# Performance work log

Hardware: AMD Instinct MI355X
Metric: run time of the kernel (lower is better)

## Reference

```python
import jax, jax.numpy as jnp
import numpy as np
from functools import partial

DIM = 192
HEADS = 8
DN = ('NCHW', 'OIHW', 'NCHW')


def conv1x1(x, w):
    # w: [O, I, 1, 1]
    return jax.lax.conv_general_dilated(x, w, (1, 1), 'VALID', dimension_numbers=DN)


def dwconv3x3(x, w):
    # w: [C, 1, 3, 3], depthwise
    return jax.lax.conv_general_dilated(x, w, (1, 1), 'SAME', dimension_numbers=DN,
                                        feature_group_count=x.shape[1])


def l2norm(x, eps=1e-12):
    n = jnp.sqrt(jnp.sum(x * x, axis=-1, keepdims=True))
    return x / jnp.maximum(n, eps)


def compute_attention(q, k_s, v_s, k_c, v_c, temperature, beta):
    b, c, h, w = q.shape
    hw = h * w
    r = lambda t: t.reshape(b, HEADS, c // HEADS, hw)  # b head c (h w)
    qn = l2norm(r(q))
    ks = l2norm(r(k_s))
    kc = l2norm(r(k_c))
    vs, vc = r(v_s), r(v_c)
    # channel-wise attention: [b, head, c, c]
    sa = jax.nn.softmax(jnp.einsum('bhcn,bhdn->bhcd', qn, ks) * temperature, axis=-1)
    so = jnp.einsum('bhcd,bhdn->bhcn', sa, vs)
    ca = jax.nn.softmax(-(jnp.einsum('bhcn,bhdn->bhcd', qn, kc) * temperature), axis=-1)
    co = jnp.einsum('bhcd,bhdn->bhcn', ca, vc)
    out = jax.nn.sigmoid(beta) * so + co
    return out.reshape(b, c, h, w)


def setup_inputs() -> dict:
    key = jax.random.key(0)
    ks = jax.random.split(key, 8)
    B, C, H, W = 8, DIM, 128, 128
    s = 0.02
    return {
        'x1': jax.random.normal(ks[0], (B, C, H, W), jnp.float32),
        'x2': jax.random.normal(ks[1], (B, C, H, W), jnp.float32),
        'w_qkv1': jax.random.normal(ks[2], (3 * C, C, 1, 1), jnp.float32) * s,
        'w_dw1': jax.random.normal(ks[3], (3 * C, 1, 3, 3), jnp.float32) * s,
        'w_qkv2': jax.random.normal(ks[4], (3 * C, C, 1, 1), jnp.float32) * s,
        'w_dw2': jax.random.normal(ks[5], (3 * C, 1, 3, 3), jnp.float32) * s,
        'w_proj': jax.random.normal(ks[6], (C, C, 1, 1), jnp.float32) * s,
        'temperature': jnp.ones((HEADS, 1, 1), jnp.float32),
        'beta': jnp.zeros((1,), jnp.float32),
    }


def reference(x1, x2, w_qkv1, w_dw1, w_qkv2, w_dw2, w_proj, temperature, beta):
    qkv1 = dwconv3x3(conv1x1(x1, w_qkv1), w_dw1)
    q1, k1, v1 = jnp.split(qkv1, 3, axis=1)
    qkv2 = dwconv3x3(conv1x1(x2, w_qkv2), w_dw2)
    q2, k2, v2 = jnp.split(qkv2, 3, axis=1)
    e1 = compute_attention(q1, k1, v1, k2, v2, temperature, beta)
    e2 = compute_attention(q2, k2, v2, k1, v1, temperature, beta)
    return conv1x1(e1, w_proj), conv1x1(e2, w_proj)
```

## Files before the change

### kernel.cpp

```cpp
#include <hip/hip_runtime.h>

typedef unsigned short u16;
typedef unsigned int u32;

#define NB 8
#define NCH 192
#define NC3 576
#define NHW 16384
#define NHEADS 8

typedef __attribute__((ext_vector_type(8))) short s16x8;
typedef __attribute__((ext_vector_type(4))) float f32x4;

__device__ __forceinline__ float bf2f(u32 h) {
  return __uint_as_float(h << 16);
}
__device__ __forceinline__ u16 f2bf(float f) {
  u32 u = __float_as_uint(f);
  u = (u + 0x7fffu + ((u >> 16) & 1u)) >> 16;
  return (u16)u;
}
__device__ __forceinline__ u32 pk2(u16 a, u16 b) { return (u32)a | ((u32)b << 16); }

__device__ __forceinline__ int swz(int row) { return ((row >> 1) & 7) << 4; }

__device__ __forceinline__ void gl_lds16(const void* g, void* s) {
  __builtin_amdgcn_global_load_lds((const __attribute__((address_space(1))) unsigned int*)g,
                                   (__attribute__((address_space(3))) unsigned int*)s, 16, 0, 0);
}

__global__ __launch_bounds__(256) void wcast_kernel(
    const float* __restrict__ w1, const float* __restrict__ w2,
    u16* __restrict__ o1, u16* __restrict__ o2, float* __restrict__ norms2) {
  int i = blockIdx.x * 256 + threadIdx.x;
  if (i < NC3 * NCH) {
    o1[i] = f2bf(w1[i]);
    o2[i] = f2bf(w2[i]);
  }
  if (i < 4 * NB * NCH) norms2[i] = 0.f;
}

__global__ __launch_bounds__(256) void conv_mfma_kernel(
    const float* __restrict__ x, const u16* __restrict__ wbf, u16* __restrict__ pre) {
  __shared__ char smem[40960];
  u16* Al = (u16*)smem;
  u16* Bl = (u16*)(smem + 24576);
  const int bid = blockIdx.x;
  const int id = (bid & 7) * 384 + (bid >> 3);
  const int b = id / 384;
  const int rr = id % 384;
  const int nbase = (rr / 3) * 128;
  const int obase = (rr % 3) * 192;
  const int tid = threadIdx.x;
  const int w = tid >> 6, l = tid & 63;
  const int wr = w >> 1, wc = w & 1;

  f32x4 acc[6][4];
#pragma unroll
  for (int m = 0; m < 6; ++m)
#pragma unroll
    for (int nf = 0; nf < 4; ++nf) acc[m][nf] = (f32x4)0.f;

  for (int kb = 0; kb < 192; kb += 64) {
#pragma unroll
    for (int i = 0; i < 6; ++i) {
      const int grp = i * 4 + w;
      const int row = grp * 8 + (l >> 3);
      const int cb = ((l & 7) * 16) ^ swz(row);
      const char* src = (const char*)wbf + (size_t)(obase + row) * 384 + kb * 2 + cb;
      gl_lds16(src, (char*)Al + grp * 1024);
    }
#pragma unroll
    for (int pi = 0; pi < 2; ++pi) {
      const int p = pi * 256 + tid;
      const int ng = p & 31, kg = p >> 5;
      const float* xr = x + (((size_t)b * NCH + kb + kg * 4) << 14) + nbase + ng * 4;
      float4 f0 = *(const float4*)(xr);
      float4 f1 = *(const float4*)(xr + NHW);
      float4 f2 = *(const float4*)(xr + 2 * NHW);
      float4 f3 = *(const float4*)(xr + 3 * NHW);
      u16 e0[4] = {f2bf(f0.x), f2bf(f0.y), f2bf(f0.z), f2bf(f0.w)};
      u16 e1[4] = {f2bf(f1.x), f2bf(f1.y), f2bf(f1.z), f2bf(f1.w)};
      u16 e2[4] = {f2bf(f2.x), f2bf(f2.y), f2bf(f2.z), f2bf(f2.w)};
      u16 e3[4] = {f2bf(f3.x), f2bf(f3.y), f2bf(f3.z), f2bf(f3.w)};
#pragma unroll
      for (int nn = 0; nn < 4; ++nn) {
        const int row = ng * 4 + nn;
        const int cb = (kg * 8) ^ swz(row);
        *(uint2*)((char*)Bl + row * 128 + cb) = make_uint2(pk2(e0[nn], e1[nn]), pk2(e2[nn], e3[nn]));
      }
    }
    __syncthreads();
#pragma unroll
    for (int kk = 0; kk < 2; ++kk) {
      s16x8 a[6], bv[4];
      const int cbk = kk * 64 + (l >> 4) * 16;
#pragma unroll
      for (int m = 0; m < 6; ++m) {
        const int rowA = wr * 96 + m * 16 + (l & 15);
        a[m] = *(const s16x8*)((const char*)Al + rowA * 128 + (cbk ^ swz(rowA)));
      }
#pragma unroll
      for (int nf = 0; nf < 4; ++nf) {
        const int rowB = wc * 64 + nf * 16 + (l & 15);
        bv[nf] = *(const s16x8*)((const char*)Bl + rowB * 128 + (cbk ^ swz(rowB)));
      }
#pragma unroll
      for (int m = 0; m < 6; ++m)
#pragma unroll
        for (int nf = 0; nf < 4; ++nf)
          acc[m][nf] = __builtin_amdgcn_mfma_f32_16x16x32_bf16(a[m], bv[nf], acc[m][nf], 0, 0, 0);
    }
    __syncthreads();
  }
  u16* cw = (u16*)(smem) + w * 16 * 72;
#pragma unroll
  for (int m = 0; m < 6; ++m) {
#pragma unroll
    for (int nf = 0; nf < 4; ++nf)
#pragma unroll
      for (int r = 0; r < 4; ++r)
        cw[((l >> 4) * 4 + r) * 72 + nf * 16 + (l & 15)] = f2bf(acc[m][nf][r]);
#pragma unroll
    for (int p = 0; p < 2; ++p) {
      const int chunk = p * 64 + l;
      const int row = chunk >> 3, cg = chunk & 7;
      uint4 v = *(const uint4*)(cw + row * 72 + cg * 8);
      const int o = obase + wr * 96 + m * 16 + row;
      const int n = nbase + wc * 64 + cg * 8;
      *(uint4*)(pre + (((size_t)b * NC3 + o) << 14) + n) = v;
    }
  }
}

__global__ __launch_bounds__(256) void dwconv_kernel(
    const u16* __restrict__ in, const float* __restrict__ wdw, u16* __restrict__ out,
    float* __restrict__ norms2, const int mod) {
  const size_t t = (size_t)blockIdx.x * 256 + threadIdx.x;
  const int tid = threadIdx.x;
  const int l = tid & 63;
  const int xc = (int)(t & 15);
  const int yy = (int)((t >> 4) & 127);
  const int bc = (int)(t >> 11);
  const int c = bc % NC3;
  const int b = bc / NC3;
  const u16* p = in + ((size_t)bc << 14);
  const float* wc = wdw + c * 9;
  const int x0 = xc * 8;

  float a[3][10];
#pragma unroll
  for (int r = 0; r < 3; ++r) {
    const int y2 = yy + r - 1;
    if ((unsigned)y2 < 128u) {
      const u16* row = p + (y2 << 7);
      uint4 v = *(const uint4*)(row + x0);
      a[r][1] = bf2f(v.x & 0xffff); a[r][2] = bf2f(v.x >> 16);
      a[r][3] = bf2f(v.y & 0xffff); a[r][4] = bf2f(v.y >> 16);
      a[r][5] = bf2f(v.z & 0xffff); a[r][6] = bf2f(v.z >> 16);
      a[r][7] = bf2f(v.w & 0xffff); a[r][8] = bf2f(v.w >> 16);
    } else {
#pragma unroll
      for (int j = 1; j < 9; ++j) a[r][j] = 0.f;
    }
    const float lf = __shfl(a[r][8], (l - 1) & 63, 64);
    const float rt = __shfl(a[r][1], (l + 1) & 63, 64);
    a[r][0] = (xc > 0) ? lf : 0.f;
    a[r][9] = (xc < 15) ? rt : 0.f;
  }
  const float w00 = wc[0], w01 = wc[1], w02 = wc[2];
  const float w10 = wc[3], w11 = wc[4], w12 = wc[5];
  const float w20 = wc[6], w21 = wc[7], w22 = wc[8];
  u16 o[8];
  float ssq = 0.f;
#pragma unroll
  for (int j = 0; j < 8; ++j) {
    float s = a[0][j] * w00;
    s = fmaf(a[0][j + 1], w01, s);
    s = fmaf(a[0][j + 2], w02, s);
    s = fmaf(a[1][j], w10, s);
    s = fmaf(a[1][j + 1], w11, s);
    s = fmaf(a[1][j + 2], w12, s);
    s = fmaf(a[2][j], w20, s);
    s = fmaf(a[2][j + 1], w21, s);
    s = fmaf(a[2][j + 2], w22, s);
    ssq = fmaf(s, s, ssq);
    o[j] = f2bf(s);
  }
  *(uint4*)(out + (t << 3)) =
      make_uint4(pk2(o[0], o[1]), pk2(o[2], o[3]), pk2(o[4], o[5]), pk2(o[6], o[7]));

  if (c < 384) {
#pragma unroll
    for (int off = 32; off > 0; off >>= 1) ssq += __shfl_down(ssq, off, 64);
    __shared__ float red[4];
    if ((tid & 63) == 0) red[tid >> 6] = ssq;
    __syncthreads();
    if (tid == 0) {
      const int tt = (c < 192) ? mod : 2 + mod;
      atomicAdd(&norms2[(tt * NB + b) * NCH + (c % NCH)], red[0] + red[1] + red[2] + red[3]);
    }
  }
}

__global__ __launch_bounds__(256) void gram_mfma_kernel(
    const u16* __restrict__ qkv1, const u16* __restrict__ qkv2, float* __restrict__ gp) {
  const int nc = blockIdx.x, h = blockIdx.y, b = blockIdx.z;
  const int tid = threadIdx.x;
  const int w = tid >> 6, l = tid & 63;

  const u16* qp[3];
  const u16* kp[3];
#pragma unroll
  for (int m = 0; m < 3; ++m) {
    const int rq = m * 16 + (l & 15);
    const int cc = h * 24 + (rq < 24 ? rq : rq - 24);
    const u16* basep = (rq < 24) ? qkv1 : qkv2;
    qp[m] = basep + (((size_t)b * NC3 + cc) << 14);
    kp[m] = basep + (((size_t)b * NC3 + 192 + cc) << 14);
  }
  const int kbase = nc * 1024 + w * 256 + (l >> 4) * 8;

  f32x4 acc[3][3];
#pragma unroll
  for (int m = 0; m < 3; ++m)
#pragma unroll
    for (int nf = 0; nf < 3; ++nf) acc[m][nf] = (f32x4)0.f;

  for (int t = 0; t < 8; ++t) {
    const int ko = kbase + t * 32;
    s16x8 a[3], bv[3];
#pragma unroll
    for (int m = 0; m < 3; ++m) {
      a[m] = *(const s16x8*)(qp[m] + ko);
      bv[m] = *(const s16x8*)(kp[m] + ko);
    }
#pragma unroll
    for (int m = 0; m < 3; ++m)
#pragma unroll
      for (int nf = 0; nf < 3; ++nf)
        acc[m][nf] = __builtin_amdgcn_mfma_f32_16x16x32_bf16(a[m], bv[nf], acc[m][nf], 0, 0, 0);
  }

  __shared__ float red[4][48][48];
#pragma unroll
  for (int m = 0; m < 3; ++m)
#pragma unroll
    for (int nf = 0; nf < 3; ++nf)
#pragma unroll
      for (int r = 0; r < 4; ++r)
        red[w][m * 16 + (l >> 4) * 4 + r][nf * 16 + (l & 15)] = acc[m][nf][r];
  __syncthreads();
  float* dst = gp + ((((size_t)b * 8 + h) * 16 + nc) * 2304);
  for (int e = tid; e < 2304; e += 256) {
    const int rr = e / 48, cc = e % 48;
    dst[e] = red[0][rr][cc] + red[1][rr][cc] + red[2][rr][cc] + red[3][rr][cc];
  }
}

__global__ __launch_bounds__(256) void gram_reduce_kernel(
    const float* __restrict__ gp, float* __restrict__ G) {
  const int bh = blockIdx.x;
  for (int e = threadIdx.x; e < 2304; e += 256) {
    float s = 0.f;
    for (int p = 0; p < 16; ++p) s += gp[((size_t)bh * 16 + p) * 2304 + e];
    G[(size_t)bh * 2304 + e] = s;
  }
}

__global__ __launch_bounds__(256) void softmax_wcat_kernel(
    const float* __restrict__ G, const float* __restrict__ norms2,
    const float* __restrict__ temperature, const float* __restrict__ beta,
    const float* __restrict__ wproj, u16* __restrict__ Wcat) {
  const int bh = blockIdx.x;
  const int b = bh >> 3, h = bh & 7;
  __shared__ float sm[4][24][24];
  __shared__ float nrm[4][24];
  const int tid = threadIdx.x;
  if (tid < 96) {
    int t = tid / 24, ci = tid % 24;
    nrm[t][ci] = fmaxf(sqrtf(norms2[(t * NB + b) * NCH + h * 24 + ci]), 1e-12f);
  }
  __syncthreads();
  const float T = temperature[h];
  const float sigB = 1.f / (1.f + expf(-beta[0]));
  if (tid < 96) {
    const int m = tid / 24, r = tid % 24;
    const float* Gb = G + (size_t)bh * 2304;
    const int gr = (m >= 2) ? 24 + r : r;
    const int gc0 = (m == 1 || m == 2) ? 24 : 0;
    const float* qn = (m >= 2) ? nrm[1] : nrm[0];
    const float* kn = (m == 1 || m == 2) ? nrm[3] : nrm[2];
    const float sign = (m == 0 || m == 2) ? 1.f : -1.f;
    const float qs = sign * T / qn[r];
    float L[24], mx = -1e30f;
#pragma unroll
    for (int cc = 0; cc < 24; ++cc) {
      L[cc] = Gb[gr * 48 + gc0 + cc] * qs / kn[cc];
      mx = fmaxf(mx, L[cc]);
    }
    float ssum = 0.f;
#pragma unroll
    for (int cc = 0; cc < 24; ++cc) {
      L[cc] = expf(L[cc] - mx);
      ssum += L[cc];
    }
    const float inv = 1.f / ssum;
#pragma unroll
    for (int cc = 0; cc < 24; ++cc) sm[m][r][cc] = L[cc] * inv;
  }
  __syncthreads();
  for (int e = tid; e < 384 * 48; e += 256) {
    const int o = e / 48, dc = e % 48;
    const int part = dc / 24, d = dc % 24;
    const int oc = (o < 192) ? o : o - 192;
    int m;
    float scale;
    if (o < 192) { m = part ? 1 : 0; scale = part ? 1.f : sigB; }
    else         { m = part ? 2 : 3; scale = part ? sigB : 1.f; }
    float s = 0.f;
#pragma unroll
    for (int ci = 0; ci < 24; ++ci) s += wproj[oc * 192 + h * 24 + ci] * sm[m][ci][d];
    Wcat[((size_t)b * 384 + o) * 384 + part * 192 + h * 24 + d] = f2bf(s * scale);
  }
}

__global__ __launch_bounds__(256) void final_mfma_kernel(
    const u16* __restrict__ qkv1, const u16* __restrict__ qkv2,
    const u16* __restrict__ Wcat, float* __restrict__ out) {
  __shared__ char smem[32768];
  u16* Al = (u16*)smem;
  u16* Bl = (u16*)(smem + 16384);
  const int bid = blockIdx.x;
  const int id = (bid & 7) * 384 + (bid >> 3);
  const int b = id / 384;
  const int rr2 = id % 384;
  const int nbase = (rr2 / 3) * 128;
  const int obase = (rr2 % 3) * 128;
  const int tid = threadIdx.x;
  const int w = tid >> 6, l = tid & 63;
  const int wr = w >> 1, wc = w & 1;

  f32x4 acc[4][4];
#pragma unroll
  for (int m = 0; m < 4; ++m)
#pragma unroll
    for (int nf = 0; nf < 4; ++nf) acc[m][nf] = (f32x4)0.f;

  for (int kb = 0; kb < 384; kb += 64) {
#pragma unroll
    for (int i = 0; i < 4; ++i) {
      const int grp = i * 4 + w;
      const int row = grp * 8 + (l >> 3);
      const int cb = ((l & 7) * 16) ^ swz(row);
      const char* src = (const char*)Wcat + ((size_t)b * 384 + obase + row) * 768 + kb * 2 + cb;
      gl_lds16(src, (char*)Al + grp * 1024);
    }
    const u16* vbase = (kb < 192) ? qkv1 + (((size_t)b * NC3 + 384 + kb) << 14)
                                  : qkv2 + (((size_t)b * NC3 + 384 + kb - 192) << 14);
#pragma unroll
    for (int pi = 0; pi < 2; ++pi) {
      const int p = pi * 256 + tid;
      const int ng = p & 31, kg = p >> 5;
      const u16* vr = vbase + (((size_t)kg * 4) << 14) + nbase + ng * 4;
      uint2 r0 = *(const uint2*)(vr);
      uint2 r1 = *(const uint2*)(vr + NHW);
      uint2 r2 = *(const uint2*)(vr + 2 * NHW);
      uint2 r3 = *(const uint2*)(vr + 3 * NHW);
      u16 e0[4] = {(u16)(r0.x & 0xffff), (u16)(r0.x >> 16), (u16)(r0.y & 0xffff), (u16)(r0.y >> 16)};
      u16 e1[4] = {(u16)(r1.x & 0xffff), (u16)(r1.x >> 16), (u16)(r1.y & 0xffff), (u16)(r1.y >> 16)};
      u16 e2[4] = {(u16)(r2.x & 0xffff), (u16)(r2.x >> 16), (u16)(r2.y & 0xffff), (u16)(r2.y >> 16)};
      u16 e3[4] = {(u16)(r3.x & 0xffff), (u16)(r3.x >> 16), (u16)(r3.y & 0xffff), (u16)(r3.y >> 16)};
#pragma unroll
      for (int nn = 0; nn < 4; ++nn) {
        const int row = ng * 4 + nn;
        const int cb = (kg * 8) ^ swz(row);
        *(uint2*)((char*)Bl + row * 128 + cb) = make_uint2(pk2(e0[nn], e1[nn]), pk2(e2[nn], e3[nn]));
      }
    }
    __syncthreads();
#pragma unroll
    for (int kk = 0; kk < 2; ++kk) {
      s16x8 a[4], bv[4];
      const int cbk = kk * 64 + (l >> 4) * 16;
#pragma unroll
      for (int m = 0; m < 4; ++m) {
        const int rowA = wr * 64 + m * 16 + (l & 15);
        a[m] = *(const s16x8*)((const char*)Al + rowA * 128 + (cbk ^ swz(rowA)));
      }
#pragma unroll
      for (int nf = 0; nf < 4; ++nf) {
        const int rowB = wc * 64 + nf * 16 + (l & 15);
        bv[nf] = *(const s16x8*)((const char*)Bl + rowB * 128 + (cbk ^ swz(rowB)));
      }
#pragma unroll
      for (int m = 0; m < 4; ++m)
#pragma unroll
        for (int nf = 0; nf < 4; ++nf)
          acc[m][nf] = __builtin_amdgcn_mfma_f32_16x16x32_bf16(a[m], bv[nf], acc[m][nf], 0, 0, 0);
    }
    __syncthreads();
  }
  float* cw = (float*)(smem + w * 4352);
#pragma unroll
  for (int m = 0; m < 4; ++m) {
#pragma unroll
    for (int nf = 0; nf < 4; ++nf)
#pragma unroll
      for (int r = 0; r < 4; ++r)
        cw[((l >> 4) * 4 + r) * 68 + nf * 16 + (l & 15)] = acc[m][nf][r];
#pragma unroll
    for (int p = 0; p < 4; ++p) {
      const int chunk = p * 64 + l;
      const int row = chunk >> 4, cg = chunk & 15;
      float4 v = *(const float4*)(cw + row * 68 + cg * 4);
      const int o = obase + wr * 64 + m * 16 + row;
      const int n = nbase + wc * 64 + cg * 4;
      float* dst = (o < 192) ? out + (((size_t)b * NCH + o) << 14) + n
                             : out + 25165824 + (((size_t)b * NCH + o - 192) << 14) + n;
      *(float4*)dst = v;
    }
  }
}

extern "C" void kernel_launch(void* const* d_in, const int* in_sizes, int n_in,
                              void* d_out, int out_size, void* d_ws, size_t ws_size,
                              hipStream_t stream) {
  (void)in_sizes; (void)n_in; (void)out_size; (void)ws_size;
  const float* x1 = (const float*)d_in[0];
  const float* x2 = (const float*)d_in[1];
  const float* w_qkv1 = (const float*)d_in[2];
  const float* w_dw1 = (const float*)d_in[3];
  const float* w_qkv2 = (const float*)d_in[4];
  const float* w_dw2 = (const float*)d_in[5];
  const float* w_proj = (const float*)d_in[6];
  const float* temperature = (const float*)d_in[7];
  const float* beta = (const float*)d_in[8];
  float* out = (float*)d_out;

  char* wsb = (char*)d_ws;
  u16* pre = (u16*)(wsb);
  u16* qkv1 = (u16*)(wsb + 150994944);
  u16* qkv2 = (u16*)(wsb + 301989888);
  u16* wbf1 = (u16*)(wsb + 452984832);
  u16* wbf2 = (u16*)(wsb + 453206016);
  float* norms2 = (float*)(wsb + 453427200);
  float* G = (float*)(wsb + 453451776);
  u16* WcatBf = (u16*)(wsb + 454041600);
  float* gp = (float*)(wsb + 456400896);

  const int dwblocks = (int)(((size_t)NB * NC3 * NHW) / (256 * 8));

  wcast_kernel<<<(NC3 * NCH + 255) / 256, 256, 0, stream>>>(w_qkv1, w_qkv2, wbf1, wbf2, norms2);
  conv_mfma_kernel<<<3072, 256, 0, stream>>>(x1, wbf1, pre);
  dwconv_kernel<<<dwblocks, 256, 0, stream>>>(pre, w_dw1, qkv1, norms2, 0);
  conv_mfma_kernel<<<3072, 256, 0, stream>>>(x2, wbf2, pre);
  dwconv_kernel<<<dwblocks, 256, 0, stream>>>(pre, w_dw2, qkv2, norms2, 1);
  gram_mfma_kernel<<<dim3(16, NHEADS, NB), 256, 0, stream>>>(qkv1, qkv2, gp);
  gram_reduce_kernel<<<NB * NHEADS, 256, 0, stream>>>(gp, G);
  softmax_wcat_kernel<<<NB * NHEADS, 256, 0, stream>>>(G, norms2, temperature, beta, w_proj, WcatBf);
  final_mfma_kernel<<<3072, 256, 0, stream>>>(qkv1, qkv2, WcatBf, out);
}
```

Baseline: 518.4 us.

## Double-buffer operand tiles in conv and final MFMA GEMM kernels

```diff
diff --git a/kernel.cpp b/kernel.cpp
--- a/kernel.cpp
+++ b/kernel.cpp
@@ -40,11 +40,53 @@
   if (i < 4 * NB * NCH) norms2[i] = 0.f;
 }
 
+__device__ __forceinline__ void conv_b_load(const float* __restrict__ x, int b, int nbase,
+                                            int kb, int tid, float4 (&fB)[2][4]) {
+#pragma unroll
+  for (int pi = 0; pi < 2; ++pi) {
+    const int p = pi * 256 + tid;
+    const int ng = p & 31, kg = p >> 5;
+    const float* xr = x + (((size_t)b * NCH + kb + kg * 4) << 14) + nbase + ng * 4;
+    fB[pi][0] = *(const float4*)(xr);
+    fB[pi][1] = *(const float4*)(xr + NHW);
+    fB[pi][2] = *(const float4*)(xr + 2 * NHW);
+    fB[pi][3] = *(const float4*)(xr + 3 * NHW);
+  }
+}
+
+__device__ __forceinline__ void conv_b_write(char* smem, int tid, const float4 (&fB)[2][4]) {
+#pragma unroll
+  for (int pi = 0; pi < 2; ++pi) {
+    const int p = pi * 256 + tid;
+    const int ng = p & 31, kg = p >> 5;
+    u16 e0[4] = {f2bf(fB[pi][0].x), f2bf(fB[pi][0].y), f2bf(fB[pi][0].z), f2bf(fB[pi][0].w)};
+    u16 e1[4] = {f2bf(fB[pi][1].x), f2bf(fB[pi][1].y), f2bf(fB[pi][1].z), f2bf(fB[pi][1].w)};
+    u16 e2[4] = {f2bf(fB[pi][2].x), f2bf(fB[pi][2].y), f2bf(fB[pi][2].z), f2bf(fB[pi][2].w)};
+    u16 e3[4] = {f2bf(fB[pi][3].x), f2bf(fB[pi][3].y), f2bf(fB[pi][3].z), f2bf(fB[pi][3].w)};
+#pragma unroll
+    for (int nn = 0; nn < 4; ++nn) {
+      const int row = ng * 4 + nn;
+      const int cb = (kg * 8) ^ swz(row);
+      *(uint2*)(smem + 49152 + row * 128 + cb) = make_uint2(pk2(e0[nn], e1[nn]), pk2(e2[nn], e3[nn]));
+    }
+  }
+}
+
+__device__ __forceinline__ void conv_a_glds(char* smem, const u16* __restrict__ wbf,
+                                            int obase, int kb, int w, int l, int buf) {
+#pragma unroll
+  for (int i = 0; i < 6; ++i) {
+    const int grp = i * 4 + w;
+    const int row = grp * 8 + (l >> 3);
+    const int cb = ((l & 7) * 16) ^ swz(row);
+    const char* src = (const char*)wbf + (size_t)(obase + row) * 384 + kb * 2 + cb;
+    gl_lds16(src, smem + buf * 24576 + grp * 1024);
+  }
+}
+
 __global__ __launch_bounds__(256) void conv_mfma_kernel(
     const float* __restrict__ x, const u16* __restrict__ wbf, u16* __restrict__ pre) {
-  __shared__ char smem[40960];
-  u16* Al = (u16*)smem;
-  u16* Bl = (u16*)(smem + 24576);
+  __shared__ char smem[65536];
   const int bid = blockIdx.x;
   const int id = (bid & 7) * 384 + (bid >> 3);
   const int b = id / 384;
@@ -61,36 +103,19 @@
 #pragma unroll
     for (int nf = 0; nf < 4; ++nf) acc[m][nf] = (f32x4)0.f;
 
-  for (int kb = 0; kb < 192; kb += 64) {
-#pragma unroll
-    for (int i = 0; i < 6; ++i) {
-      const int grp = i * 4 + w;
-      const int row = grp * 8 + (l >> 3);
-      const int cb = ((l & 7) * 16) ^ swz(row);
-      const char* src = (const char*)wbf + (size_t)(obase + row) * 384 + kb * 2 + cb;
-      gl_lds16(src, (char*)Al + grp * 1024);
-    }
-#pragma unroll
-    for (int pi = 0; pi < 2; ++pi) {
-      const int p = pi * 256 + tid;
-      const int ng = p & 31, kg = p >> 5;
-      const float* xr = x + (((size_t)b * NCH + kb + kg * 4) << 14) + nbase + ng * 4;
-      float4 f0 = *(const float4*)(xr);
-      float4 f1 = *(const float4*)(xr + NHW);
-      float4 f2 = *(const float4*)(xr + 2 * NHW);
-      float4 f3 = *(const float4*)(xr + 3 * NHW);
-      u16 e0[4] = {f2bf(f0.x), f2bf(f0.y), f2bf(f0.z), f2bf(f0.w)};
-      u16 e1[4] = {f2bf(f1.x), f2bf(f1.y), f2bf(f1.z), f2bf(f1.w)};
-      u16 e2[4] = {f2bf(f2.x), f2bf(f2.y), f2bf(f2.z), f2bf(f2.w)};
-      u16 e3[4] = {f2bf(f3.x), f2bf(f3.y), f2bf(f3.z), f2bf(f3.w)};
-#pragma unroll
-      for (int nn = 0; nn < 4; ++nn) {
-        const int row = ng * 4 + nn;
-        const int cb = (kg * 8) ^ swz(row);
-        *(uint2*)((char*)Bl + row * 128 + cb) = make_uint2(pk2(e0[nn], e1[nn]), pk2(e2[nn], e3[nn]));
-      }
-    }
-    __syncthreads();
+  float4 fB[2][4];
+  conv_b_load(x, b, nbase, 0, tid, fB);
+  conv_a_glds(smem, wbf, obase, 0, w, l, 0);
+  conv_b_write(smem, tid, fB);
+  __syncthreads();
+
+  for (int t = 0; t < 3; ++t) {
+    const int cur = t & 1;
+    const int nxt = cur ^ 1;
+    if (t < 2) {
+      conv_b_load(x, b, nbase, (t + 1) * 64, tid, fB);
+      conv_a_glds(smem, wbf, obase, (t + 1) * 64, w, l, nxt);
+    }
 #pragma unroll
     for (int kk = 0; kk < 2; ++kk) {
       s16x8 a[6], bv[4];
@@ -98,12 +123,12 @@
 #pragma unroll
       for (int m = 0; m < 6; ++m) {
         const int rowA = wr * 96 + m * 16 + (l & 15);
-        a[m] = *(const s16x8*)((const char*)Al + rowA * 128 + (cbk ^ swz(rowA)));
+        a[m] = *(const s16x8*)(smem + cur * 24576 + rowA * 128 + (cbk ^ swz(rowA)));
       }
 #pragma unroll
       for (int nf = 0; nf < 4; ++nf) {
         const int rowB = wc * 64 + nf * 16 + (l & 15);
-        bv[nf] = *(const s16x8*)((const char*)Bl + rowB * 128 + (cbk ^ swz(rowB)));
+        bv[nf] = *(const s16x8*)(smem + 49152 + rowB * 128 + (cbk ^ swz(rowB)));
       }
 #pragma unroll
       for (int m = 0; m < 6; ++m)
@@ -112,6 +137,10 @@
           acc[m][nf] = __builtin_amdgcn_mfma_f32_16x16x32_bf16(a[m], bv[nf], acc[m][nf], 0, 0, 0);
     }
     __syncthreads();
+    if (t < 2) {
+      conv_b_write(smem, tid, fB);
+      __syncthreads();
+    }
   }
   u16* cw = (u16*)(smem) + w * 16 * 72;
 #pragma unroll
@@ -325,12 +354,60 @@
   }
 }
 
+__device__ __forceinline__ void fin_b_load(const u16* __restrict__ qkv1,
+                                           const u16* __restrict__ qkv2,
+                                           int b, int nbase, int kb, int tid,
+                                           uint2 (&fV)[2][4]) {
+  const u16* vbase = (kb < 192) ? qkv1 + (((size_t)b * NC3 + 384 + kb) << 14)
+                                : qkv2 + (((size_t)b * NC3 + 384 + kb - 192) << 14);
+#pragma unroll
+  for (int pi = 0; pi < 2; ++pi) {
+    const int p = pi * 256 + tid;
+    const int ng = p & 31, kg = p >> 5;
+    const u16* vr = vbase + (((size_t)kg * 4) << 14) + nbase + ng * 4;
+    fV[pi][0] = *(const uint2*)(vr);
+    fV[pi][1] = *(const uint2*)(vr + NHW);
+    fV[pi][2] = *(const uint2*)(vr + 2 * NHW);
+    fV[pi][3] = *(const uint2*)(vr + 3 * NHW);
+  }
+}
+
+__device__ __forceinline__ void fin_b_write(char* smem, int tid, int buf,
+                                            const uint2 (&fV)[2][4]) {
+#pragma unroll
+  for (int pi = 0; pi < 2; ++pi) {
+    const int p = pi * 256 + tid;
+    const int ng = p & 31, kg = p >> 5;
+    u16 e0[4] = {(u16)(fV[pi][0].x & 0xffff), (u16)(fV[pi][0].x >> 16), (u16)(fV[pi][0].y & 0xffff), (u16)(fV[pi][0].y >> 16)};
+    u16 e1[4] = {(u16)(fV[pi][1].x & 0xffff), (u16)(fV[pi][1].x >> 16), (u16)(fV[pi][1].y & 0xffff), (u16)(fV[pi][1].y >> 16)};
+    u16 e2[4] = {(u16)(fV[pi][2].x & 0xffff), (u16)(fV[pi][2].x >> 16), (u16)(fV[pi][2].y & 0xffff), (u16)(fV[pi][2].y >> 16)};
+    u16 e3[4] = {(u16)(fV[pi][3].x & 0xffff), (u16)(fV[pi][3].x >> 16), (u16)(fV[pi][3].y & 0xffff), (u16)(fV[pi][3].y >> 16)};
+#pragma unroll
+    for (int nn = 0; nn < 4; ++nn) {
+      const int row = ng * 4 + nn;
+      const int cb = (kg * 8) ^ swz(row);
+      *(uint2*)(smem + 32768 + buf * 16384 + row * 128 + cb) =
+          make_uint2(pk2(e0[nn], e1[nn]), pk2(e2[nn], e3[nn]));
+    }
+  }
+}
+
+__device__ __forceinline__ void fin_a_glds(char* smem, const u16* __restrict__ Wcat,
+                                           int b, int obase, int kb, int w, int l, int buf) {
+#pragma unroll
+  for (int i = 0; i < 4; ++i) {
+    const int grp = i * 4 + w;
+    const int row = grp * 8 + (l >> 3);
+    const int cb = ((l & 7) * 16) ^ swz(row);
+    const char* src = (const char*)Wcat + ((size_t)b * 384 + obase + row) * 768 + kb * 2 + cb;
+    gl_lds16(src, smem + buf * 16384 + grp * 1024);
+  }
+}
+
 __global__ __launch_bounds__(256) void final_mfma_kernel(
     const u16* __restrict__ qkv1, const u16* __restrict__ qkv2,
     const u16* __restrict__ Wcat, float* __restrict__ out) {
-  __shared__ char smem[32768];
-  u16* Al = (u16*)smem;
-  u16* Bl = (u16*)(smem + 16384);
+  __shared__ char smem[65536];
   const int bid = blockIdx.x;
   const int id = (bid & 7) * 384 + (bid >> 3);
   const int b = id / 384;
@@ -347,38 +424,19 @@
 #pragma unroll
     for (int nf = 0; nf < 4; ++nf) acc[m][nf] = (f32x4)0.f;
 
-  for (int kb = 0; kb < 384; kb += 64) {
-#pragma unroll
-    for (int i = 0; i < 4; ++i) {
-      const int grp = i * 4 + w;
-      const int row = grp * 8 + (l >> 3);
-      const int cb = ((l & 7) * 16) ^ swz(row);
-      const char* src = (const char*)Wcat + ((size_t)b * 384 + obase + row) * 768 + kb * 2 + cb;
-      gl_lds16(src, (char*)Al + grp * 1024);
-    }
-    const u16* vbase = (kb < 192) ? qkv1 + (((size_t)b * NC3 + 384 + kb) << 14)
-                                  : qkv2 + (((size_t)b * NC3 + 384 + kb - 192) << 14);
-#pragma unroll
-    for (int pi = 0; pi < 2; ++pi) {
-      const int p = pi * 256 + tid;
-      const int ng = p & 31, kg = p >> 5;
-      const u16* vr = vbase + (((size_t)kg * 4) << 14) + nbase + ng * 4;
-      uint2 r0 = *(const uint2*)(vr);
-      uint2 r1 = *(const uint2*)(vr + NHW);
-      uint2 r2 = *(const uint2*)(vr + 2 * NHW);
-      uint2 r3 = *(const uint2*)(vr + 3 * NHW);
-      u16 e0[4] = {(u16)(r0.x & 0xffff), (u16)(r0.x >> 16), (u16)(r0.y & 0xffff), (u16)(r0.y >> 16)};
-      u16 e1[4] = {(u16)(r1.x & 0xffff), (u16)(r1.x >> 16), (u16)(r1.y & 0xffff), (u16)(r1.y >> 16)};
-      u16 e2[4] = {(u16)(r2.x & 0xffff), (u16)(r2.x >> 16), (u16)(r2.y & 0xffff), (u16)(r2.y >> 16)};
-      u16 e3[4] = {(u16)(r3.x & 0xffff), (u16)(r3.x >> 16), (u16)(r3.y & 0xffff), (u16)(r3.y >> 16)};
-#pragma unroll
-      for (int nn = 0; nn < 4; ++nn) {
-        const int row = ng * 4 + nn;
-        const int cb = (kg * 8) ^ swz(row);
-        *(uint2*)((char*)Bl + row * 128 + cb) = make_uint2(pk2(e0[nn], e1[nn]), pk2(e2[nn], e3[nn]));
-      }
-    }
-    __syncthreads();
+  uint2 fV[2][4];
+  fin_b_load(qkv1, qkv2, b, nbase, 0, tid, fV);
+  fin_a_glds(smem, Wcat, b, obase, 0, w, l, 0);
+  fin_b_write(smem, tid, 0, fV);
+  __syncthreads();
+
+  for (int t = 0; t < 6; ++t) {
+    const int cur = t & 1;
+    const int nxt = cur ^ 1;
+    if (t < 5) {
+      fin_b_load(qkv1, qkv2, b, nbase, (t + 1) * 64, tid, fV);
+      fin_a_glds(smem, Wcat, b, obase, (t + 1) * 64, w, l, nxt);
+    }
 #pragma unroll
     for (int kk = 0; kk < 2; ++kk) {
       s16x8 a[4], bv[4];
@@ -386,12 +444,12 @@
 #pragma unroll
       for (int m = 0; m < 4; ++m) {
         const int rowA = wr * 64 + m * 16 + (l & 15);
-        a[m] = *(const s16x8*)((const char*)Al + rowA * 128 + (cbk ^ swz(rowA)));
+        a[m] = *(const s16x8*)(smem + cur * 16384 + rowA * 128 + (cbk ^ swz(rowA)));
       }
 #pragma unroll
       for (int nf = 0; nf < 4; ++nf) {
         const int rowB = wc * 64 + nf * 16 + (l & 15);
-        bv[nf] = *(const s16x8*)((const char*)Bl + rowB * 128 + (cbk ^ swz(rowB)));
+        bv[nf] = *(const s16x8*)(smem + 32768 + cur * 16384 + rowB * 128 + (cbk ^ swz(rowB)));
       }
 #pragma unroll
       for (int m = 0; m < 4; ++m)
@@ -399,6 +457,7 @@
         for (int nf = 0; nf < 4; ++nf)
           acc[m][nf] = __builtin_amdgcn_mfma_f32_16x16x32_bf16(a[m], bv[nf], acc[m][nf], 0, 0, 0);
     }
+    if (t < 5) fin_b_write(smem, tid, nxt, fV);
     __syncthreads();
   }
   float* cw = (float*)(smem + w * 4352);
```

Measured after the change: 517.4 us. No clear change (-0.2%).
